# Kernel tuning notes

Measured on AMD Instinct MI355X. Metric: run time of the kernel, lower is better.

## Reference

```python
import jax, jax.numpy as jnp
import numpy as np

BETA = 5.5
MEM_FILLED = 25  # number of occupied slots per class; remaining slots are zero (empty)


def setup_inputs() -> dict:
    key = jax.random.key(0)
    ks = jax.random.split(key, 7)
    C, M, D = 1000, 50, 1024
    mem = jax.random.normal(ks[0], (C, M, D), jnp.float32)
    # emulate a partially-filled memory bank: slots >= MEM_FILLED are empty (all-zero rows)
    mem = mem * (jnp.arange(M)[None, :, None] < MEM_FILLED)
    return {
        "img_feat": jax.random.normal(ks[1], (1, D), jnp.float32),
        "image_feature_memory": mem,
        "fixed_global_feat_vanilla": jax.random.normal(ks[2], (C, 1, D), jnp.float32),
        "global_bias": 0.01 * jax.random.normal(ks[3], (C, D), jnp.float32),
        "global_bias_key": 0.01 * jax.random.normal(ks[4], (C, D), jnp.float32),
        "global_bias_value": 0.01 * jax.random.normal(ks[5], (C, D), jnp.float32),
        "global_ffn_bias": 0.01 * jax.random.normal(ks[6], (C, D), jnp.float32),
        "logit_scale": jnp.asarray(np.log(100.0), dtype=jnp.float32),
    }


def _l2norm(x, axis=-1):
    return x / jnp.linalg.norm(x, axis=axis, keepdims=True)


def reference(img_feat, image_feature_memory, fixed_global_feat_vanilla,
              global_bias, global_bias_key, global_bias_value,
              global_ffn_bias, logit_scale):
    # DualMem.get_image_pred, args.position == 'all', similarity_weighted classifier
    sg = jax.lax.stop_gradient  # torch.no_grad() block
    mem = jnp.concatenate([image_feature_memory, fixed_global_feat_vanilla], axis=1)  # (C, M+1, D)

    q = img_feat + jnp.mean(global_bias, axis=0, keepdims=True)      # (1, D)
    K = mem + global_bias_key[:, None, :]                             # (C, M+1, D)
    V = mem + global_bias_value[:, None, :]                           # (C, M+1, D)

    empty = (jnp.sum(mem, axis=-1) == 0)[..., None]                   # (C, M+1, 1) empty slots
    Kn = jnp.where(empty, 0.0, _l2norm(K))
    Vn = jnp.where(empty, 0.0, _l2norm(V))
    qn = _l2norm(q)
    qn, Kn, Vn = sg(qn), sg(Kn), sg(Vn)

    sim = jnp.exp(-BETA * (1.0 - jnp.einsum('d,cmd->cm', qn[0], Kn)))  # (C, M+1)
    adaptive = jnp.einsum('cm,cmd->cd', sim, Vn)                       # (C, D)
    adaptive = _l2norm(adaptive)
    adaptive = adaptive[None] + global_ffn_bias[None]                  # (1, C, D) position in {'output','all'}
    adaptive = _l2norm(adaptive)

    logits = jnp.exp(logit_scale) * jnp.einsum('bcd,bd->bc', adaptive, img_feat)  # (1, C)
    return jax.nn.softmax(logits, axis=1)
```

## Files before the change

### kernel.cpp

```cpp
#include <hip/hip_runtime.h>
#include <math.h>

#define BETA 5.5f
#define NC 1000
#define NM 51
#define ND 1024

typedef float nt_float4 __attribute__((ext_vector_type(4)));

__device__ __forceinline__ float wave_reduce_sum(float v) {
#pragma unroll
    for (int off = 32; off >= 1; off >>= 1) v += __shfl_xor(v, off, 64);
    return v;
}

__device__ __forceinline__ float block_reduce_sum(float v, float* red, int w, int lane) {
    v = wave_reduce_sum(v);
    __syncthreads();
    if (lane == 0) red[w] = v;
    __syncthreads();
    return red[0] + red[1] + red[2] + red[3];
}

__global__ __launch_bounds__(128) void colsum_kernel(const float* __restrict__ gb,
                                                     float* __restrict__ qpart) {
    int d = blockIdx.x * 128 + threadIdx.x;
    int c0 = blockIdx.y * 125;
    const float* p = gb + (size_t)c0 * ND + d;
    float s = 0.f;
    for (int c = 0; c < 125; ++c) s += p[(size_t)c * ND];
    qpart[blockIdx.y * ND + d] = s;
}

__global__ __launch_bounds__(256) void dualmem_main(
    const float* __restrict__ img,
    const float* __restrict__ mem,
    const float* __restrict__ fixedg,
    const float* __restrict__ qpart,
    const float* __restrict__ gbk,
    const float* __restrict__ gbv,
    float* __restrict__ accpart)
{
    __shared__ float lds_acc[4 * ND];

    const int c = blockIdx.x >> 1;
    const int half = blockIdx.x & 1;
    const int t = threadIdx.x;
    const int w = t >> 6;
    const int lane = t & 63;
    const int ww = half * 4 + w;

    float4 qn[4];
    float ssq = 0.f;
#pragma unroll
    for (int j = 0; j < 4; ++j) {
        float4 sv = make_float4(0.f, 0.f, 0.f, 0.f);
#pragma unroll
        for (int p = 0; p < 8; ++p) {
            float4 pv = ((const float4*)qpart)[p * 256 + j * 64 + lane];
            sv.x += pv.x; sv.y += pv.y; sv.z += pv.z; sv.w += pv.w;
        }
        float4 iv = ((const float4*)img)[j * 64 + lane];
        float4 qv;
        qv.x = iv.x + sv.x * (1.f / NC);
        qv.y = iv.y + sv.y * (1.f / NC);
        qv.z = iv.z + sv.z * (1.f / NC);
        qv.w = iv.w + sv.w * (1.f / NC);
        ssq += qv.x * qv.x + qv.y * qv.y + qv.z * qv.z + qv.w * qv.w;
        qn[j] = qv;
    }
    ssq = wave_reduce_sum(ssq);
    float qrn = rsqrtf(ssq);
#pragma unroll
    for (int j = 0; j < 4; ++j) {
        qn[j].x *= qrn; qn[j].y *= qrn; qn[j].z *= qrn; qn[j].w *= qrn;
    }

    const float* bkp = gbk + (size_t)c * ND;
    const float* bvp = gbv + (size_t)c * ND;
    float4 bk[4], bv[4], acc[4];
#pragma unroll
    for (int j = 0; j < 4; ++j) {
        bk[j] = ((const float4*)bkp)[j * 64 + lane];
        bv[j] = ((const float4*)bvp)[j * 64 + lane];
        acc[j] = make_float4(0.f, 0.f, 0.f, 0.f);
    }

    for (int m = ww; m < NM; m += 8) {
        const nt_float4* row = (m < 50) ? (const nt_float4*)(mem + ((size_t)c * 50 + m) * ND)
                                        : (const nt_float4*)(fixedg + (size_t)c * ND);
        nt_float4 mv[4];
        float sm = 0.f, ssqK = 0.f, dotK = 0.f, ssqV = 0.f;
#pragma unroll
        for (int j = 0; j < 4; ++j) {
            nt_float4 v = __builtin_nontemporal_load(&row[j * 64 + lane]);
            mv[j] = v;
            sm += v.x + v.y + v.z + v.w;
            float kx = v.x + bk[j].x, ky = v.y + bk[j].y, kz = v.z + bk[j].z, kw = v.w + bk[j].w;
            ssqK += kx * kx + ky * ky + kz * kz + kw * kw;
            dotK += qn[j].x * kx + qn[j].y * ky + qn[j].z * kz + qn[j].w * kw;
            float vx = v.x + bv[j].x, vy = v.y + bv[j].y, vz = v.z + bv[j].z, vw = v.w + bv[j].w;
            ssqV += vx * vx + vy * vy + vz * vz + vw * vw;
        }
        sm   = wave_reduce_sum(sm);
        ssqK = wave_reduce_sum(ssqK);
        dotK = wave_reduce_sum(dotK);
        ssqV = wave_reduce_sum(ssqV);
        if (sm != 0.f) {
            float simv = expf(-BETA * (1.f - dotK * rsqrtf(ssqK)));
            float wt = simv * rsqrtf(ssqV);
#pragma unroll
            for (int j = 0; j < 4; ++j) {
                acc[j].x += wt * (mv[j].x + bv[j].x);
                acc[j].y += wt * (mv[j].y + bv[j].y);
                acc[j].z += wt * (mv[j].z + bv[j].z);
                acc[j].w += wt * (mv[j].w + bv[j].w);
            }
        }
    }

#pragma unroll
    for (int j = 0; j < 4; ++j)
        ((float4*)lds_acc)[w * 256 + j * 64 + lane] = acc[j];
    __syncthreads();

    float4 a = make_float4(0.f, 0.f, 0.f, 0.f);
#pragma unroll
    for (int wv = 0; wv < 4; ++wv) {
        float4 p = ((float4*)lds_acc)[wv * 256 + t];
        a.x += p.x; a.y += p.y; a.z += p.z; a.w += p.w;
    }
    ((float4*)(accpart + (size_t)blockIdx.x * ND))[t] = a;
}

__global__ __launch_bounds__(256) void finalize_kernel(
    const float* __restrict__ img,
    const float* __restrict__ accpart,
    const float* __restrict__ ffn,
    const float* __restrict__ lsp,
    float* __restrict__ logits)
{
    __shared__ float red[8];
    const int c = blockIdx.x;
    const int t = threadIdx.x;
    const int w = t >> 6;
    const int lane = t & 63;

    float4 a0 = ((const float4*)(accpart + (size_t)(2 * c) * ND))[t];
    float4 a1 = ((const float4*)(accpart + (size_t)(2 * c + 1) * ND))[t];
    float4 a;
    a.x = a0.x + a1.x; a.y = a0.y + a1.y; a.z = a0.z + a1.z; a.w = a0.w + a1.w;

    float ssqA = block_reduce_sum(a.x * a.x + a.y * a.y + a.z * a.z + a.w * a.w, red, w, lane);
    float arn = rsqrtf(ssqA);
    float4 fv = ((const float4*)(ffn + (size_t)c * ND))[t];
    a.x = a.x * arn + fv.x;
    a.y = a.y * arn + fv.y;
    a.z = a.z * arn + fv.z;
    a.w = a.w * arn + fv.w;
    float ssqB = block_reduce_sum(a.x * a.x + a.y * a.y + a.z * a.z + a.w * a.w, red, w, lane);
    float brn = rsqrtf(ssqB);

    float4 iv = ((const float4*)img)[t];
    float dp = a.x * iv.x + a.y * iv.y + a.z * iv.z + a.w * iv.w;
    dp = block_reduce_sum(dp, red, w, lane);

    if (t == 0) logits[c] = expf(lsp[0]) * dp * brn;
}

__global__ __launch_bounds__(256) void softmax_kernel(const float* __restrict__ logits,
                                                      float* __restrict__ out) {
    __shared__ float red[8];
    int t = threadIdx.x, w = t >> 6, lane = t & 63;
    float l[4];
#pragma unroll
    for (int i = 0; i < 4; ++i) {
        int idx = t * 4 + i;
        l[i] = (idx < NC) ? logits[idx] : -3.402823466e+38f;
    }
    float mx = fmaxf(fmaxf(l[0], l[1]), fmaxf(l[2], l[3]));
#pragma unroll
    for (int off = 32; off >= 1; off >>= 1) mx = fmaxf(mx, __shfl_xor(mx, off, 64));
    __syncthreads();
    if (lane == 0) red[w] = mx;
    __syncthreads();
    mx = fmaxf(fmaxf(red[0], red[1]), fmaxf(red[2], red[3]));
    __syncthreads();

    float e[4], s = 0.f;
#pragma unroll
    for (int i = 0; i < 4; ++i) {
        int idx = t * 4 + i;
        e[i] = (idx < NC) ? expf(l[i] - mx) : 0.f;
        s += e[i];
    }
    s = block_reduce_sum(s, red, w, lane);
    float inv = 1.f / s;
#pragma unroll
    for (int i = 0; i < 4; ++i) {
        int idx = t * 4 + i;
        if (idx < NC) out[idx] = e[i] * inv;
    }
}

extern "C" void kernel_launch(void* const* d_in, const int* in_sizes, int n_in,
                              void* d_out, int out_size, void* d_ws, size_t ws_size,
                              hipStream_t stream) {
    const float* img    = (const float*)d_in[0];
    const float* mem    = (const float*)d_in[1];
    const float* fixedg = (const float*)d_in[2];
    const float* gb     = (const float*)d_in[3];
    const float* gbk    = (const float*)d_in[4];
    const float* gbv    = (const float*)d_in[5];
    const float* ffn    = (const float*)d_in[6];
    const float* ls     = (const float*)d_in[7];

    float* ws      = (float*)d_ws;
    float* qpart   = ws;
    float* accpart = ws + 8 * ND;
    float* logits  = accpart + 2000 * ND;
    float* out     = (float*)d_out;

    colsum_kernel<<<dim3(8, 8), 128, 0, stream>>>(gb, qpart);
    dualmem_main<<<2 * NC, 256, 0, stream>>>(img, mem, fixedg, qpart, gbk, gbv, accpart);
    finalize_kernel<<<NC, 256, 0, stream>>>(img, accpart, ffn, ls, logits);
    softmax_kernel<<<1, 256, 0, stream>>>(logits, out);
}
```

Measured before the change: 320.1 us.

## Precompute normalized query in separate kernel and prefetch next memory row

The column sum of global_bias is split across 40 blocks of vectorized float4 loads, and a new single-block kernel normalizes the query once, instead of every dualmem block re-reducing the partial sums. The main loop now double-buffers memory rows in registers, issuing the next row's nontemporal loads before processing the current one. The aim is to hide load latency in the bandwidth-bound main kernel and remove redundant per-block query work. It costs one extra launch plus more live registers, which could reduce occupancy.

```diff
diff --git a/kernel.cpp b/kernel.cpp
--- a/kernel.cpp
+++ b/kernel.cpp
@@ -22,21 +22,46 @@
     return red[0] + red[1] + red[2] + red[3];
 }
 
-__global__ __launch_bounds__(128) void colsum_kernel(const float* __restrict__ gb,
-                                                     float* __restrict__ qpart) {
-    int d = blockIdx.x * 128 + threadIdx.x;
-    int c0 = blockIdx.y * 125;
-    const float* p = gb + (size_t)c0 * ND + d;
-    float s = 0.f;
-    for (int c = 0; c < 125; ++c) s += p[(size_t)c * ND];
-    qpart[blockIdx.y * ND + d] = s;
+__global__ __launch_bounds__(256) void colsum_part(const float* __restrict__ gb,
+                                                   float* __restrict__ qpart) {
+    const int t = threadIdx.x;
+    const float4* p = (const float4*)(gb + (size_t)blockIdx.x * 25 * ND) + t;
+    float4 s = make_float4(0.f, 0.f, 0.f, 0.f);
+#pragma unroll
+    for (int c = 0; c < 25; ++c) {
+        float4 v = p[c * (ND / 4)];
+        s.x += v.x; s.y += v.y; s.z += v.z; s.w += v.w;
+    }
+    ((float4*)qpart)[blockIdx.x * (ND / 4) + t] = s;
+}
+
+__global__ __launch_bounds__(256) void qnorm_kernel(const float* __restrict__ img,
+                                                    const float* __restrict__ qpart,
+                                                    float* __restrict__ qn) {
+    __shared__ float red[8];
+    const int t = threadIdx.x, w = t >> 6, lane = t & 63;
+    float4 s = make_float4(0.f, 0.f, 0.f, 0.f);
+#pragma unroll
+    for (int p = 0; p < 40; ++p) {
+        float4 v = ((const float4*)qpart)[p * (ND / 4) + t];
+        s.x += v.x; s.y += v.y; s.z += v.z; s.w += v.w;
+    }
+    float4 iv = ((const float4*)img)[t];
+    float4 q;
+    q.x = iv.x + s.x * (1.f / NC);
+    q.y = iv.y + s.y * (1.f / NC);
+    q.z = iv.z + s.z * (1.f / NC);
+    q.w = iv.w + s.w * (1.f / NC);
+    float ssq = block_reduce_sum(q.x * q.x + q.y * q.y + q.z * q.z + q.w * q.w, red, w, lane);
+    float r = rsqrtf(ssq);
+    float4 o = make_float4(q.x * r, q.y * r, q.z * r, q.w * r);
+    ((float4*)qn)[t] = o;
 }
 
 __global__ __launch_bounds__(256) void dualmem_main(
-    const float* __restrict__ img,
     const float* __restrict__ mem,
     const float* __restrict__ fixedg,
-    const float* __restrict__ qpart,
+    const float* __restrict__ qn_g,
     const float* __restrict__ gbk,
     const float* __restrict__ gbv,
     float* __restrict__ accpart)
@@ -50,51 +75,38 @@
     const int lane = t & 63;
     const int ww = half * 4 + w;
 
-    float4 qn[4];
-    float ssq = 0.f;
-#pragma unroll
-    for (int j = 0; j < 4; ++j) {
-        float4 sv = make_float4(0.f, 0.f, 0.f, 0.f);
-#pragma unroll
-        for (int p = 0; p < 8; ++p) {
-            float4 pv = ((const float4*)qpart)[p * 256 + j * 64 + lane];
-            sv.x += pv.x; sv.y += pv.y; sv.z += pv.z; sv.w += pv.w;
-        }
-        float4 iv = ((const float4*)img)[j * 64 + lane];
-        float4 qv;
-        qv.x = iv.x + sv.x * (1.f / NC);
-        qv.y = iv.y + sv.y * (1.f / NC);
-        qv.z = iv.z + sv.z * (1.f / NC);
-        qv.w = iv.w + sv.w * (1.f / NC);
-        ssq += qv.x * qv.x + qv.y * qv.y + qv.z * qv.z + qv.w * qv.w;
-        qn[j] = qv;
-    }
-    ssq = wave_reduce_sum(ssq);
-    float qrn = rsqrtf(ssq);
-#pragma unroll
-    for (int j = 0; j < 4; ++j) {
-        qn[j].x *= qrn; qn[j].y *= qrn; qn[j].z *= qrn; qn[j].w *= qrn;
-    }
-
+    float4 qn[4], bk[4], bv[4], acc[4];
     const float* bkp = gbk + (size_t)c * ND;
     const float* bvp = gbv + (size_t)c * ND;
-    float4 bk[4], bv[4], acc[4];
 #pragma unroll
     for (int j = 0; j < 4; ++j) {
+        qn[j] = ((const float4*)qn_g)[j * 64 + lane];
         bk[j] = ((const float4*)bkp)[j * 64 + lane];
         bv[j] = ((const float4*)bvp)[j * 64 + lane];
         acc[j] = make_float4(0.f, 0.f, 0.f, 0.f);
     }
 
+    nt_float4 cur[4], nxt[4];
+    {
+        const nt_float4* r = (ww < 50) ? (const nt_float4*)(mem + ((size_t)c * 50 + ww) * ND)
+                                       : (const nt_float4*)(fixedg + (size_t)c * ND);
+#pragma unroll
+        for (int j = 0; j < 4; ++j) cur[j] = __builtin_nontemporal_load(&r[j * 64 + lane]);
+    }
+
     for (int m = ww; m < NM; m += 8) {
-        const nt_float4* row = (m < 50) ? (const nt_float4*)(mem + ((size_t)c * 50 + m) * ND)
-                                        : (const nt_float4*)(fixedg + (size_t)c * ND);
-        nt_float4 mv[4];
+        const int mn = m + 8;
+        if (mn < NM) {
+            const nt_float4* r = (mn < 50) ? (const nt_float4*)(mem + ((size_t)c * 50 + mn) * ND)
+                                           : (const nt_float4*)(fixedg + (size_t)c * ND);
+#pragma unroll
+            for (int j = 0; j < 4; ++j) nxt[j] = __builtin_nontemporal_load(&r[j * 64 + lane]);
+        }
+
         float sm = 0.f, ssqK = 0.f, dotK = 0.f, ssqV = 0.f;
 #pragma unroll
         for (int j = 0; j < 4; ++j) {
-            nt_float4 v = __builtin_nontemporal_load(&row[j * 64 + lane]);
-            mv[j] = v;
+            nt_float4 v = cur[j];
             sm += v.x + v.y + v.z + v.w;
             float kx = v.x + bk[j].x, ky = v.y + bk[j].y, kz = v.z + bk[j].z, kw = v.w + bk[j].w;
             ssqK += kx * kx + ky * ky + kz * kz + kw * kw;
@@ -111,12 +123,14 @@
             float wt = simv * rsqrtf(ssqV);
 #pragma unroll
             for (int j = 0; j < 4; ++j) {
-                acc[j].x += wt * (mv[j].x + bv[j].x);
-                acc[j].y += wt * (mv[j].y + bv[j].y);
-                acc[j].z += wt * (mv[j].z + bv[j].z);
-                acc[j].w += wt * (mv[j].w + bv[j].w);
+                acc[j].x += wt * (cur[j].x + bv[j].x);
+                acc[j].y += wt * (cur[j].y + bv[j].y);
+                acc[j].z += wt * (cur[j].z + bv[j].z);
+                acc[j].w += wt * (cur[j].w + bv[j].w);
             }
         }
+#pragma unroll
+        for (int j = 0; j < 4; ++j) cur[j] = nxt[j];
     }
 
 #pragma unroll
@@ -217,12 +231,14 @@
 
     float* ws      = (float*)d_ws;
     float* qpart   = ws;
-    float* accpart = ws + 8 * ND;
+    float* qn      = ws + 40 * ND;
+    float* accpart = ws + 41 * ND;
     float* logits  = accpart + 2000 * ND;
     float* out     = (float*)d_out;
 
-    colsum_kernel<<<dim3(8, 8), 128, 0, stream>>>(gb, qpart);
-    dualmem_main<<<2 * NC, 256, 0, stream>>>(img, mem, fixedg, qpart, gbk, gbv, accpart);
+    colsum_part<<<40, 256, 0, stream>>>(gb, qpart);
+    qnorm_kernel<<<1, 256, 0, stream>>>(img, qpart, qn);
+    dualmem_main<<<2 * NC, 256, 0, stream>>>(mem, fixedg, qn, gbk, gbv, accpart);
     finalize_kernel<<<NC, 256, 0, stream>>>(img, accpart, ffn, ls, logits);
     softmax_kernel<<<1, 256, 0, stream>>>(logits, out);
 }
```

After: 303.1 us. 1.06x faster.
